# Performance work log

Measured on AMD Instinct MI355X. Metric: run time of the kernel, lower is better.

Reference implementation:

```python
import jax, jax.numpy as jnp
import numpy as np

N = 50000
E = 640000
NFEAT = 128
NHID = 128
ALPHA = 0.2  # leaky relu slope


def setup_inputs() -> dict:
    key = jax.random.key(0)
    k1, k2, k3, k4, k5 = jax.random.split(key, 5)
    x = jax.random.normal(k1, (N, NFEAT), dtype=jnp.float32)
    W = jax.random.normal(k2, (NFEAT, NHID), dtype=jnp.float32) * (1.0 / np.sqrt(NFEAT))
    a = jax.random.normal(k3, (1, 2 * NHID), dtype=jnp.float32) * 0.1
    # every node appears at least once as a source so rowsum > 0 (as in a real adjacency)
    src = jnp.concatenate([jnp.arange(N, dtype=jnp.int64 if jax.config.read('jax_enable_x64') else jnp.int32),
                           jax.random.randint(k4, (E - N,), 0, N)]).astype(jnp.int32)
    dst = jax.random.randint(k5, (E,), 0, N).astype(jnp.int32)
    edge_index = jnp.stack([src, dst], axis=0)
    return {"x": x, "W": W, "a": a, "edge_index": edge_index, "no_need_param": 0}


def reference(x, W, a, edge_index, no_need_param):
    # SpGraphAttentionLayer (concat=False), single head
    h = x @ W                                   # [N, nhid]
    src, dst = edge_index[0], edge_index[1]     # [E]
    nhid = W.shape[1]
    a1, a2 = a[0, :nhid], a[0, nhid:]
    # a @ cat(h[src], h[dst])  ==  h[src]@a1 + h[dst]@a2
    score = h[src] @ a1 + h[dst] @ a2           # [E]
    e = jnp.exp(-jax.nn.leaky_relu(score, ALPHA))
    n = x.shape[0]
    rowsum = jax.ops.segment_sum(e, src, num_segments=n)              # [N]
    h_prime = jax.ops.segment_sum(e[:, None] * h[dst], src, num_segments=n)  # [N, nhid]
    neighborhood_emb = h_prime / (rowsum[:, None] + 1e-16)
    # fused combine: elu(x @ W - neighborhood aggregation)
    mapped_fea = x @ W
    return jax.nn.elu(mapped_fea - neighborhood_emb)
```

## Files before the change

### kernel.cpp

```cpp
#include <hip/hip_runtime.h>
#include <hip/hip_fp16.h>
#include <math.h>

#define NFEAT 128
#define NHID  128
#define ALPHA 0.2f

typedef __attribute__((ext_vector_type(8))) short short8;
typedef __attribute__((ext_vector_type(4))) float f32x4;

__device__ inline unsigned int pack_bf16x2_rn(float x, float y) {
    unsigned int bx = __float_as_uint(x), by = __float_as_uint(y);
    bx += 0x7fffu + ((bx >> 16) & 1u);
    by += 0x7fffu + ((by >> 16) & 1u);
    return (bx >> 16) | (by & 0xffff0000u);
}

union Frag { unsigned int u[4]; uint4 v; short8 s; };

__global__ __launch_bounds__(256) void prep_wt_kernel(
    const float* __restrict__ W, unsigned int* __restrict__ Wtg)
{
    __shared__ float tile[32][33];
    const int t  = threadIdx.x;
    const int kt = blockIdx.x >> 2;
    const int nt = blockIdx.x & 3;

    {
        const int r = t >> 3, c = t & 7;
        const float4 v = *((const float4*)&W[(size_t)(kt * 32 + r) * NHID + nt * 32 + c * 4]);
        tile[r][c * 4 + 0] = v.x; tile[r][c * 4 + 1] = v.y;
        tile[r][c * 4 + 2] = v.z; tile[r][c * 4 + 3] = v.w;
    }
    __syncthreads();

    const int nn = t & 31;
    #pragma unroll
    for (int i = 0; i < 2; ++i) {
        const int kk = (t >> 5) * 2 + i;
        Wtg[(size_t)(nt * 32 + nn) * 64 + kt * 16 + kk] =
            pack_bf16x2_rn(tile[kk * 2][nn], tile[kk * 2 + 1][nn]);
    }
}

__global__ __launch_bounds__(256) void gemm_h_kernel(
    const float* __restrict__ x, const unsigned int* __restrict__ Wtg,
    const float* __restrict__ a, float* __restrict__ h,
    unsigned int* __restrict__ hbu,
    float* __restrict__ s1, float* __restrict__ s2, int n,
    const int* __restrict__ ei, int* __restrict__ hist, int E, int gemm_blocks)
{
    __shared__ unsigned int Wtu[128 * 64];

    const int t = threadIdx.x;

    if (blockIdx.x >= gemm_blocks) {
        const int E4   = E >> 2;
        const int nthr = (gridDim.x - gemm_blocks) << 8;
        const int g    = (blockIdx.x - gemm_blocks) * 256 + t;
        for (int idx = g; idx < E4; idx += nthr) {
            const int4 s4 = ((const int4*)ei)[idx];
            atomicAdd(&hist[s4.x], 1);
            atomicAdd(&hist[s4.y], 1);
            atomicAdd(&hist[s4.z], 1);
            atomicAdd(&hist[s4.w], 1);
        }
        for (int j = (E4 << 2) + g; j < E; j += nthr) atomicAdd(&hist[ei[j]], 1);
        return;
    }

    #pragma unroll
    for (int i = 0; i < 8; ++i) {
        const int u  = i * 256 + t;
        const uint4 v = ((const uint4*)Wtg)[u];
        const int nn = u >> 4, kc = u & 15;
        *((uint4*)&Wtu[nn * 64 + (kc ^ (nn & 15)) * 4]) = v;
    }

    const int w    = t >> 6;
    const int lane = t & 63;
    const int c    = lane & 15;
    const int quad = lane >> 4;

    const int rowbase = blockIdx.x * 64 + w * 16;

    int arow = rowbase + c; if (arow >= n) arow = n - 1;
    const float4* xp = (const float4*)(x + (size_t)arow * NFEAT);
    float4 xv[8];
    #pragma unroll
    for (int s = 0; s < 4; ++s) {
        xv[2 * s]     = xp[s * 8 + quad * 2];
        xv[2 * s + 1] = xp[s * 8 + quad * 2 + 1];
    }

    float a1v[8], a2v[8];
    #pragma unroll
    for (int tt = 0; tt < 8; ++tt) {
        a1v[tt] = a[tt * 16 + c];
        a2v[tt] = a[NHID + tt * 16 + c];
    }

    f32x4 acc[8];
    #pragma unroll
    for (int tt = 0; tt < 8; ++tt) acc[tt] = (f32x4){0.f, 0.f, 0.f, 0.f};

    __syncthreads();

    #pragma unroll
    for (int s = 0; s < 4; ++s) {
        Frag afr;
        afr.u[0] = pack_bf16x2_rn(xv[2 * s].x,     xv[2 * s].y);
        afr.u[1] = pack_bf16x2_rn(xv[2 * s].z,     xv[2 * s].w);
        afr.u[2] = pack_bf16x2_rn(xv[2 * s + 1].x, xv[2 * s + 1].y);
        afr.u[3] = pack_bf16x2_rn(xv[2 * s + 1].z, xv[2 * s + 1].w);
        const int kc = s * 4 + quad;
        #pragma unroll
        for (int tt = 0; tt < 8; ++tt) {
            Frag bfr;
            bfr.v = *((const uint4*)&Wtu[(tt * 16 + c) * 64 + (kc ^ c) * 4]);
            acc[tt] = __builtin_amdgcn_mfma_f32_16x16x32_bf16(
                afr.s, bfr.s, acc[tt], 0, 0, 0);
        }
    }

    #pragma unroll
    for (int r = 0; r < 4; ++r) {
        const int  row = rowbase + quad * 4 + r;
        const bool ok  = (row < n);
        float p1 = 0.f, p2 = 0.f;
        #pragma unroll
        for (int tt = 0; tt < 8; ++tt) {
            const float v = acc[tt][r];
            if (ok) h[(size_t)row * NHID + tt * 16 + c] = v;
            p1 = fmaf(v, a1v[tt], p1);
            p2 = fmaf(v, a2v[tt], p2);
        }
        #pragma unroll
        for (int p = 0; p < 4; ++p) {
            if (ok) hbu[(size_t)row * 64 + p * 16 + c] =
                pack_bf16x2_rn(acc[2 * p][r], acc[2 * p + 1][r]);
        }
        #pragma unroll
        for (int off = 1; off <= 8; off <<= 1) {
            p1 += __shfl_xor(p1, off, 64);
            p2 += __shfl_xor(p2, off, 64);
        }
        if (ok && c == 0) { s1[row] = p1; s2[row] = p2; }
    }
}

__global__ __launch_bounds__(256) void scan_block_kernel(
    const int* __restrict__ in, int* __restrict__ out, int* __restrict__ bsums, int n)
{
    __shared__ int s[256];
    const int tid = threadIdx.x;
    const int gid = blockIdx.x * 256 + tid;
    const int v = (gid < n) ? in[gid] : 0;
    s[tid] = v;
    __syncthreads();
    #pragma unroll
    for (int off = 1; off < 256; off <<= 1) {
        const int t2 = (tid >= off) ? s[tid - off] : 0;
        __syncthreads();
        s[tid] += t2;
        __syncthreads();
    }
    if (gid < n) out[gid] = s[tid] - v;
    if (tid == 255 && bsums) bsums[blockIdx.x] = s[255];
}

__global__ __launch_bounds__(256) void scan_add_kernel(
    int* __restrict__ row_ptr, int* __restrict__ cursor,
    const int* __restrict__ bsums_scan, int n, int E)
{
    const int gid = blockIdx.x * 256 + threadIdx.x;
    if (gid < n) {
        const int v = row_ptr[gid] + bsums_scan[gid >> 8];
        row_ptr[gid] = v;
        cursor[gid]  = v;
    }
    if (gid == 0) row_ptr[n] = E;
}

__global__ __launch_bounds__(256) void scatter_kernel(
    const int* __restrict__ ei, const float* __restrict__ s1,
    const float* __restrict__ s2, int* __restrict__ cursor,
    unsigned int* __restrict__ erec, int E)
{
    const int j = blockIdx.x * 256 + threadIdx.x;
    if (j >= E) return;
    const int src = ei[j];
    const int dst = ei[E + j];
    float s = s1[src] + s2[dst];
    s = (s > 0.f) ? s : ALPHA * s;
    const float ev = expf(-s);
    const unsigned int evh = (unsigned int)__half_as_ushort(__float2half(ev));
    const int pos = atomicAdd(&cursor[src], 1);
    erec[pos] = ((unsigned int)dst << 16) | evh;
}

__global__ __launch_bounds__(256) void aggregate_kernel(
    const int* __restrict__ row_ptr, const unsigned int* __restrict__ erec,
    const unsigned int* __restrict__ hbu, const float* __restrict__ h,
    float* __restrict__ out, int n)
{
    const int node = blockIdx.x * 16 + (threadIdx.x >> 4);
    const int l    = threadIdx.x & 15;
    if (node >= n) return;

    const int beg = row_ptr[node];
    const int end = row_ptr[node + 1];

    float acc[8];
    #pragma unroll
    for (int i = 0; i < 8; ++i) acc[i] = 0.f;
    float rs = 0.f;

    #define BL(x) __uint_as_float((x) << 16)
    #define BH(x) __uint_as_float((x) & 0xffff0000u)
    #define ACC4(u, ev)                                   \
        acc[0] = fmaf(ev, BL(u.x), acc[0]);               \
        acc[4] = fmaf(ev, BH(u.x), acc[4]);               \
        acc[1] = fmaf(ev, BL(u.y), acc[1]);               \
        acc[5] = fmaf(ev, BH(u.y), acc[5]);               \
        acc[2] = fmaf(ev, BL(u.z), acc[2]);               \
        acc[6] = fmaf(ev, BH(u.z), acc[6]);               \
        acc[3] = fmaf(ev, BL(u.w), acc[3]);               \
        acc[7] = fmaf(ev, BH(u.w), acc[7]);

    int e = beg;
    for (; e + 8 <= end; e += 8) {
        unsigned int rr[8];
        uint4 u[8];
        #pragma unroll
        for (int i = 0; i < 8; ++i) rr[i] = erec[e + i];
        #pragma unroll
        for (int i = 0; i < 8; ++i)
            u[i] = ((const uint4*)(hbu + (size_t)(rr[i] >> 16) * 64))[l];
        #pragma unroll
        for (int i = 0; i < 8; ++i) {
            const float ev = __half2float(__ushort_as_half((unsigned short)(rr[i] & 0xffffu)));
            ACC4(u[i], ev);
            rs += ev;
        }
    }
    for (; e + 2 <= end; e += 2) {
        const unsigned int r0 = erec[e], r1 = erec[e + 1];
        const uint4 u0 = ((const uint4*)(hbu + (size_t)(r0 >> 16) * 64))[l];
        const uint4 u1 = ((const uint4*)(hbu + (size_t)(r1 >> 16) * 64))[l];
        const float e0 = __half2float(__ushort_as_half((unsigned short)(r0 & 0xffffu)));
        const float e1 = __half2float(__ushort_as_half((unsigned short)(r1 & 0xffffu)));
        ACC4(u0, e0); ACC4(u1, e1);
        rs += e0 + e1;
    }
    if (e < end) {
        const unsigned int r0 = erec[e];
        const uint4 u0 = ((const uint4*)(hbu + (size_t)(r0 >> 16) * 64))[l];
        const float e0 = __half2float(__ushort_as_half((unsigned short)(r0 & 0xffffu)));
        ACC4(u0, e0);
        rs += e0;
    }
    #undef ACC4
    #undef BL
    #undef BH

    const float rinv = 1.0f / (rs + 1e-16f);
    const int p = l >> 2, q = l & 3;
    const float4* hp4 = (const float4*)(h + (size_t)node * NHID);
    const float4 ha = hp4[8 * p + q];
    const float4 hb = hp4[8 * p + 4 + q];
    float4 oa, ob;
    float z;
    z = ha.x - acc[0] * rinv; oa.x = (z > 0.f) ? z : (expf(z) - 1.f);
    z = ha.y - acc[1] * rinv; oa.y = (z > 0.f) ? z : (expf(z) - 1.f);
    z = ha.z - acc[2] * rinv; oa.z = (z > 0.f) ? z : (expf(z) - 1.f);
    z = ha.w - acc[3] * rinv; oa.w = (z > 0.f) ? z : (expf(z) - 1.f);
    z = hb.x - acc[4] * rinv; ob.x = (z > 0.f) ? z : (expf(z) - 1.f);
    z = hb.y - acc[5] * rinv; ob.y = (z > 0.f) ? z : (expf(z) - 1.f);
    z = hb.z - acc[6] * rinv; ob.z = (z > 0.f) ? z : (expf(z) - 1.f);
    z = hb.w - acc[7] * rinv; ob.w = (z > 0.f) ? z : (expf(z) - 1.f);
    float4* op = (float4*)(out + (size_t)node * NHID);
    op[8 * p + q]     = oa;
    op[8 * p + 4 + q] = ob;
}

extern "C" void kernel_launch(void* const* d_in, const int* in_sizes, int n_in,
                              void* d_out, int out_size, void* d_ws, size_t ws_size,
                              hipStream_t stream) {
    const float* x  = (const float*)d_in[0];
    const float* W  = (const float*)d_in[1];
    const float* a  = (const float*)d_in[2];
    const int*   ei = (const int*)d_in[3];

    const int n = in_sizes[0] / NFEAT;
    const int E = in_sizes[3] / 2;
    const int nb = (n + 255) / 256;

    float* out = (float*)d_out;

    float*        h     = (float*)d_ws;
    unsigned int* hbu   = (unsigned int*)(h + (size_t)n * NHID);
    float*        s1    = (float*)(hbu + (size_t)n * 64);
    float*        s2    = s1 + n;
    unsigned int* erec  = (unsigned int*)(s2 + n);
    unsigned int* Wtg   = erec + E;
    int*          hist  = (int*)(Wtg + 8192);
    int*          bsums = hist + n;
    int*          bsums_scan = bsums + 256;
    int*          row_ptr    = bsums_scan + 256;
    int*          cursor     = row_ptr + (n + 1);

    hipMemsetAsync(hist, 0, ((size_t)n + 256) * sizeof(int), stream);

    prep_wt_kernel<<<16, 256, 0, stream>>>(W, Wtg);

    const int gemm_blocks = (n + 63) / 64;
    const int hist_blocks = 128;
    gemm_h_kernel<<<gemm_blocks + hist_blocks, 256, 0, stream>>>(
        x, Wtg, a, h, hbu, s1, s2, n, ei, hist, E, gemm_blocks);

    scan_block_kernel<<<nb, 256, 0, stream>>>(hist, row_ptr, bsums, n);
    scan_block_kernel<<<1, 256, 0, stream>>>(bsums, bsums_scan, nullptr, 256);
    scan_add_kernel<<<nb, 256, 0, stream>>>(row_ptr, cursor, bsums_scan, n, E);

    scatter_kernel<<<(E + 255) / 256, 256, 0, stream>>>(ei, s1, s2, cursor, erec, E);

    aggregate_kernel<<<(n + 15) / 16, 256, 0, stream>>>(row_ptr, erec, hbu, h, out, n);
}
```

Measured before the change: 180.6 us.

## Fold memset into prep kernel, merge scans, aggregate two nodes per group

Replaces the hipMemsetAsync of the histogram with extra blocks in the weight-prep kernel and folds the second-level scan into scan_add, so each block rescans the block sums itself. This removes two launches from the chain. The aggregate kernel now has each 16-lane group handle two adjacent nodes in lockstep, four edges at a time, to get more gathers in flight per thread. The cost is predicated loads and wasted work when the two nodes' degrees differ, plus higher register pressure.

```diff
diff --git a/kernel.cpp b/kernel.cpp
--- a/kernel.cpp
+++ b/kernel.cpp
@@ -19,10 +19,23 @@
 union Frag { unsigned int u[4]; uint4 v; short8 s; };
 
 __global__ __launch_bounds__(256) void prep_wt_kernel(
-    const float* __restrict__ W, unsigned int* __restrict__ Wtg)
-{
+    const float* __restrict__ W, unsigned int* __restrict__ Wtg,
+    int* __restrict__ hist, int n)
+{
+    const int t = threadIdx.x;
+
+    if (blockIdx.x >= 16) {
+        const int n4     = n >> 2;
+        const int stride = (gridDim.x - 16) << 8;
+        int4* h4 = (int4*)hist;
+        for (int i = (blockIdx.x - 16) * 256 + t; i < n4; i += stride)
+            h4[i] = make_int4(0, 0, 0, 0);
+        for (int i = (n4 << 2) + (blockIdx.x - 16) * 256 + t; i < n; i += stride)
+            hist[i] = 0;
+        return;
+    }
+
     __shared__ float tile[32][33];
-    const int t  = threadIdx.x;
     const int kt = blockIdx.x >> 2;
     const int nt = blockIdx.x & 3;
 
@@ -166,16 +179,28 @@
         __syncthreads();
     }
     if (gid < n) out[gid] = s[tid] - v;
-    if (tid == 255 && bsums) bsums[blockIdx.x] = s[255];
+    if (tid == 255) bsums[blockIdx.x] = s[255];
 }
 
 __global__ __launch_bounds__(256) void scan_add_kernel(
     int* __restrict__ row_ptr, int* __restrict__ cursor,
-    const int* __restrict__ bsums_scan, int n, int E)
-{
-    const int gid = blockIdx.x * 256 + threadIdx.x;
+    const int* __restrict__ bsums, int n, int E, int nb)
+{
+    __shared__ int s[256];
+    const int tid = threadIdx.x;
+    s[tid] = (tid < nb) ? bsums[tid] : 0;
+    __syncthreads();
+    #pragma unroll
+    for (int off = 1; off < 256; off <<= 1) {
+        const int t2 = (tid >= off) ? s[tid - off] : 0;
+        __syncthreads();
+        s[tid] += t2;
+        __syncthreads();
+    }
+    const int offset = (blockIdx.x == 0) ? 0 : s[blockIdx.x - 1];
+    const int gid = blockIdx.x * 256 + tid;
     if (gid < n) {
-        const int v = row_ptr[gid] + bsums_scan[gid >> 8];
+        const int v = row_ptr[gid] + offset;
         row_ptr[gid] = v;
         cursor[gid]  = v;
     }
@@ -204,21 +229,30 @@
     const unsigned int* __restrict__ hbu, const float* __restrict__ h,
     float* __restrict__ out, int n)
 {
-    const int node = blockIdx.x * 16 + (threadIdx.x >> 4);
-    const int l    = threadIdx.x & 15;
-    if (node >= n) return;
-
-    const int beg = row_ptr[node];
-    const int end = row_ptr[node + 1];
-
-    float acc[8];
-    #pragma unroll
-    for (int i = 0; i < 8; ++i) acc[i] = 0.f;
-    float rs = 0.f;
+    const int grp = (blockIdx.x * 256 + threadIdx.x) >> 4;
+    const int l   = threadIdx.x & 15;
+    const int nodeA = grp * 2;
+    const int nodeB = nodeA + 1;
+    if (nodeA >= n) return;
+
+    const int begA = row_ptr[nodeA];
+    const int endA = row_ptr[nodeA + 1];
+    int begB = 0, endB = 0;
+    if (nodeB < n) { begB = endA; endB = row_ptr[nodeB + 1]; }
+
+    float accA[8], accB[8];
+    #pragma unroll
+    for (int i = 0; i < 8; ++i) { accA[i] = 0.f; accB[i] = 0.f; }
+    float rsA = 0.f, rsB = 0.f;
+
+    const uint4* hbu4 = (const uint4*)hbu;
+
+    const int dA = endA - begA, dB = endB - begB;
+    const int iters = max((dA + 3) >> 2, (dB + 3) >> 2);
 
     #define BL(x) __uint_as_float((x) << 16)
     #define BH(x) __uint_as_float((x) & 0xffff0000u)
-    #define ACC4(u, ev)                                   \
+    #define ACC4(acc, u, ev)                              \
         acc[0] = fmaf(ev, BL(u.x), acc[0]);               \
         acc[4] = fmaf(ev, BH(u.x), acc[4]);               \
         acc[1] = fmaf(ev, BL(u.y), acc[1]);               \
@@ -228,60 +262,72 @@
         acc[3] = fmaf(ev, BL(u.w), acc[3]);               \
         acc[7] = fmaf(ev, BH(u.w), acc[7]);
 
-    int e = beg;
-    for (; e + 8 <= end; e += 8) {
-        unsigned int rr[8];
-        uint4 u[8];
-        #pragma unroll
-        for (int i = 0; i < 8; ++i) rr[i] = erec[e + i];
-        #pragma unroll
-        for (int i = 0; i < 8; ++i)
-            u[i] = ((const uint4*)(hbu + (size_t)(rr[i] >> 16) * 64))[l];
-        #pragma unroll
-        for (int i = 0; i < 8; ++i) {
-            const float ev = __half2float(__ushort_as_half((unsigned short)(rr[i] & 0xffffu)));
-            ACC4(u[i], ev);
-            rs += ev;
-        }
-    }
-    for (; e + 2 <= end; e += 2) {
-        const unsigned int r0 = erec[e], r1 = erec[e + 1];
-        const uint4 u0 = ((const uint4*)(hbu + (size_t)(r0 >> 16) * 64))[l];
-        const uint4 u1 = ((const uint4*)(hbu + (size_t)(r1 >> 16) * 64))[l];
-        const float e0 = __half2float(__ushort_as_half((unsigned short)(r0 & 0xffffu)));
-        const float e1 = __half2float(__ushort_as_half((unsigned short)(r1 & 0xffffu)));
-        ACC4(u0, e0); ACC4(u1, e1);
-        rs += e0 + e1;
-    }
-    if (e < end) {
-        const unsigned int r0 = erec[e];
-        const uint4 u0 = ((const uint4*)(hbu + (size_t)(r0 >> 16) * 64))[l];
-        const float e0 = __half2float(__ushort_as_half((unsigned short)(r0 & 0xffffu)));
-        ACC4(u0, e0);
-        rs += e0;
+    for (int it = 0; it < iters; ++it) {
+        const int bA = begA + it * 4;
+        const int bB = begB + it * 4;
+        unsigned int rA[4], rB[4];
+        #pragma unroll
+        for (int j = 0; j < 4; ++j) rA[j] = (bA + j < endA) ? erec[bA + j] : 0u;
+        #pragma unroll
+        for (int j = 0; j < 4; ++j) rB[j] = (bB + j < endB) ? erec[bB + j] : 0u;
+        uint4 uA[4], uB[4];
+        #pragma unroll
+        for (int j = 0; j < 4; ++j) uA[j] = hbu4[(size_t)(rA[j] >> 16) * 16 + l];
+        #pragma unroll
+        for (int j = 0; j < 4; ++j) uB[j] = hbu4[(size_t)(rB[j] >> 16) * 16 + l];
+        #pragma unroll
+        for (int j = 0; j < 4; ++j) {
+            const float evA = __half2float(__ushort_as_half((unsigned short)(rA[j] & 0xffffu)));
+            const float evB = __half2float(__ushort_as_half((unsigned short)(rB[j] & 0xffffu)));
+            ACC4(accA, uA[j], evA);
+            ACC4(accB, uB[j], evB);
+            rsA += evA; rsB += evB;
+        }
     }
     #undef ACC4
     #undef BL
     #undef BH
 
-    const float rinv = 1.0f / (rs + 1e-16f);
     const int p = l >> 2, q = l & 3;
-    const float4* hp4 = (const float4*)(h + (size_t)node * NHID);
-    const float4 ha = hp4[8 * p + q];
-    const float4 hb = hp4[8 * p + 4 + q];
-    float4 oa, ob;
-    float z;
-    z = ha.x - acc[0] * rinv; oa.x = (z > 0.f) ? z : (expf(z) - 1.f);
-    z = ha.y - acc[1] * rinv; oa.y = (z > 0.f) ? z : (expf(z) - 1.f);
-    z = ha.z - acc[2] * rinv; oa.z = (z > 0.f) ? z : (expf(z) - 1.f);
-    z = ha.w - acc[3] * rinv; oa.w = (z > 0.f) ? z : (expf(z) - 1.f);
-    z = hb.x - acc[4] * rinv; ob.x = (z > 0.f) ? z : (expf(z) - 1.f);
-    z = hb.y - acc[5] * rinv; ob.y = (z > 0.f) ? z : (expf(z) - 1.f);
-    z = hb.z - acc[6] * rinv; ob.z = (z > 0.f) ? z : (expf(z) - 1.f);
-    z = hb.w - acc[7] * rinv; ob.w = (z > 0.f) ? z : (expf(z) - 1.f);
-    float4* op = (float4*)(out + (size_t)node * NHID);
-    op[8 * p + q]     = oa;
-    op[8 * p + 4 + q] = ob;
+
+    {
+        const float rinv = 1.0f / (rsA + 1e-16f);
+        const float4* hp4 = (const float4*)(h + (size_t)nodeA * NHID);
+        const float4 ha = hp4[8 * p + q];
+        const float4 hb = hp4[8 * p + 4 + q];
+        float4 oa, ob;
+        float z;
+        z = ha.x - accA[0] * rinv; oa.x = (z > 0.f) ? z : (expf(z) - 1.f);
+        z = ha.y - accA[1] * rinv; oa.y = (z > 0.f) ? z : (expf(z) - 1.f);
+        z = ha.z - accA[2] * rinv; oa.z = (z > 0.f) ? z : (expf(z) - 1.f);
+        z = ha.w - accA[3] * rinv; oa.w = (z > 0.f) ? z : (expf(z) - 1.f);
+        z = hb.x - accA[4] * rinv; ob.x = (z > 0.f) ? z : (expf(z) - 1.f);
+        z = hb.y - accA[5] * rinv; ob.y = (z > 0.f) ? z : (expf(z) - 1.f);
+        z = hb.z - accA[6] * rinv; ob.z = (z > 0.f) ? z : (expf(z) - 1.f);
+        z = hb.w - accA[7] * rinv; ob.w = (z > 0.f) ? z : (expf(z) - 1.f);
+        float4* op = (float4*)(out + (size_t)nodeA * NHID);
+        op[8 * p + q]     = oa;
+        op[8 * p + 4 + q] = ob;
+    }
+    if (nodeB < n) {
+        const float rinv = 1.0f / (rsB + 1e-16f);
+        const float4* hp4 = (const float4*)(h + (size_t)nodeB * NHID);
+        const float4 ha = hp4[8 * p + q];
+        const float4 hb = hp4[8 * p + 4 + q];
+        float4 oa, ob;
+        float z;
+        z = ha.x - accB[0] * rinv; oa.x = (z > 0.f) ? z : (expf(z) - 1.f);
+        z = ha.y - accB[1] * rinv; oa.y = (z > 0.f) ? z : (expf(z) - 1.f);
+        z = ha.z - accB[2] * rinv; oa.z = (z > 0.f) ? z : (expf(z) - 1.f);
+        z = ha.w - accB[3] * rinv; oa.w = (z > 0.f) ? z : (expf(z) - 1.f);
+        z = hb.x - accB[4] * rinv; ob.x = (z > 0.f) ? z : (expf(z) - 1.f);
+        z = hb.y - accB[5] * rinv; ob.y = (z > 0.f) ? z : (expf(z) - 1.f);
+        z = hb.z - accB[6] * rinv; ob.z = (z > 0.f) ? z : (expf(z) - 1.f);
+        z = hb.w - accB[7] * rinv; ob.w = (z > 0.f) ? z : (expf(z) - 1.f);
+        float4* op = (float4*)(out + (size_t)nodeB * NHID);
+        op[8 * p + q]     = oa;
+        op[8 * p + 4 + q] = ob;
+    }
 }
 
 extern "C" void kernel_launch(void* const* d_in, const int* in_sizes, int n_in,
@@ -306,13 +352,10 @@
     unsigned int* Wtg   = erec + E;
     int*          hist  = (int*)(Wtg + 8192);
     int*          bsums = hist + n;
-    int*          bsums_scan = bsums + 256;
-    int*          row_ptr    = bsums_scan + 256;
-    int*          cursor     = row_ptr + (n + 1);
-
-    hipMemsetAsync(hist, 0, ((size_t)n + 256) * sizeof(int), stream);
-
-    prep_wt_kernel<<<16, 256, 0, stream>>>(W, Wtg);
+    int*          row_ptr = bsums + 256;
+    int*          cursor  = row_ptr + (n + 1);
+
+    prep_wt_kernel<<<16 + 50, 256, 0, stream>>>(W, Wtg, hist, n);
 
     const int gemm_blocks = (n + 63) / 64;
     const int hist_blocks = 128;
@@ -320,10 +363,11 @@
         x, Wtg, a, h, hbu, s1, s2, n, ei, hist, E, gemm_blocks);
 
     scan_block_kernel<<<nb, 256, 0, stream>>>(hist, row_ptr, bsums, n);
-    scan_block_kernel<<<1, 256, 0, stream>>>(bsums, bsums_scan, nullptr, 256);
-    scan_add_kernel<<<nb, 256, 0, stream>>>(row_ptr, cursor, bsums_scan, n, E);
+    scan_add_kernel<<<nb, 256, 0, stream>>>(row_ptr, cursor, bsums, n, E, nb);
 
     scatter_kernel<<<(E + 255) / 256, 256, 0, stream>>>(ei, s1, s2, cursor, erec, E);
 
-    aggregate_kernel<<<(n + 15) / 16, 256, 0, stream>>>(row_ptr, erec, hbu, h, out, n);
-}
+    const int groups = (n + 1) / 2;
+    aggregate_kernel<<<(groups * 16 + 255) / 256, 256, 0, stream>>>(
+        row_ptr, erec, hbu, h, out, n);
+}
```

Result: no change. 182.9 us (+1.3%).

## Drop fp32 h buffer, fold memset and bsums scan into other kernels

Applied to the files above, without the earlier changes.

Stops writing the fp32 h matrix and instead reads the bf16 copy for the final subtraction, which removes about 25MB of writes plus reads. The hist zeroing moves from a memset into extra blocks of the prep kernel. The separate single-block scan of block sums is merged into scan_add, where every block redoes that small scan. The hbu layout changes to one uint4 store per row per lane. These steps remove two launches and a lot of memory traffic, at the cost of lower precision (bf16) for the x@W term in the output.

```diff
diff --git a/kernel.cpp b/kernel.cpp
--- a/kernel.cpp
+++ b/kernel.cpp
@@ -19,10 +19,23 @@
 union Frag { unsigned int u[4]; uint4 v; short8 s; };
 
 __global__ __launch_bounds__(256) void prep_wt_kernel(
-    const float* __restrict__ W, unsigned int* __restrict__ Wtg)
-{
+    const float* __restrict__ W, unsigned int* __restrict__ Wtg,
+    int* __restrict__ hist, int n)
+{
+    const int t = threadIdx.x;
+
+    if (blockIdx.x >= 16) {
+        const int n4     = n >> 2;
+        const int stride = (gridDim.x - 16) << 8;
+        int4* h4 = (int4*)hist;
+        for (int i = (blockIdx.x - 16) * 256 + t; i < n4; i += stride)
+            h4[i] = make_int4(0, 0, 0, 0);
+        for (int i = (n4 << 2) + (blockIdx.x - 16) * 256 + t; i < n; i += stride)
+            hist[i] = 0;
+        return;
+    }
+
     __shared__ float tile[32][33];
-    const int t  = threadIdx.x;
     const int kt = blockIdx.x >> 2;
     const int nt = blockIdx.x & 3;
 
@@ -45,8 +58,7 @@
 
 __global__ __launch_bounds__(256) void gemm_h_kernel(
     const float* __restrict__ x, const unsigned int* __restrict__ Wtg,
-    const float* __restrict__ a, float* __restrict__ h,
-    unsigned int* __restrict__ hbu,
+    const float* __restrict__ a, unsigned int* __restrict__ hbu,
     float* __restrict__ s1, float* __restrict__ s2, int n,
     const int* __restrict__ ei, int* __restrict__ hist, int E, int gemm_blocks)
 {
@@ -131,14 +143,16 @@
         #pragma unroll
         for (int tt = 0; tt < 8; ++tt) {
             const float v = acc[tt][r];
-            if (ok) h[(size_t)row * NHID + tt * 16 + c] = v;
             p1 = fmaf(v, a1v[tt], p1);
             p2 = fmaf(v, a2v[tt], p2);
         }
-        #pragma unroll
-        for (int p = 0; p < 4; ++p) {
-            if (ok) hbu[(size_t)row * 64 + p * 16 + c] =
-                pack_bf16x2_rn(acc[2 * p][r], acc[2 * p + 1][r]);
+        if (ok) {
+            uint4 pk;
+            pk.x = pack_bf16x2_rn(acc[0][r], acc[1][r]);
+            pk.y = pack_bf16x2_rn(acc[2][r], acc[3][r]);
+            pk.z = pack_bf16x2_rn(acc[4][r], acc[5][r]);
+            pk.w = pack_bf16x2_rn(acc[6][r], acc[7][r]);
+            *((uint4*)&hbu[(size_t)row * 64 + c * 4]) = pk;
         }
         #pragma unroll
         for (int off = 1; off <= 8; off <<= 1) {
@@ -166,16 +180,28 @@
         __syncthreads();
     }
     if (gid < n) out[gid] = s[tid] - v;
-    if (tid == 255 && bsums) bsums[blockIdx.x] = s[255];
+    if (tid == 255) bsums[blockIdx.x] = s[255];
 }
 
 __global__ __launch_bounds__(256) void scan_add_kernel(
     int* __restrict__ row_ptr, int* __restrict__ cursor,
-    const int* __restrict__ bsums_scan, int n, int E)
-{
-    const int gid = blockIdx.x * 256 + threadIdx.x;
+    const int* __restrict__ bsums, int n, int E, int nb)
+{
+    __shared__ int s[256];
+    const int tid = threadIdx.x;
+    s[tid] = (tid < nb) ? bsums[tid] : 0;
+    __syncthreads();
+    #pragma unroll
+    for (int off = 1; off < 256; off <<= 1) {
+        const int t2 = (tid >= off) ? s[tid - off] : 0;
+        __syncthreads();
+        s[tid] += t2;
+        __syncthreads();
+    }
+    const int offset = (blockIdx.x == 0) ? 0 : s[blockIdx.x - 1];
+    const int gid = blockIdx.x * 256 + tid;
     if (gid < n) {
-        const int v = row_ptr[gid] + bsums_scan[gid >> 8];
+        const int v = row_ptr[gid] + offset;
         row_ptr[gid] = v;
         cursor[gid]  = v;
     }
@@ -201,10 +227,9 @@
 
 __global__ __launch_bounds__(256) void aggregate_kernel(
     const int* __restrict__ row_ptr, const unsigned int* __restrict__ erec,
-    const unsigned int* __restrict__ hbu, const float* __restrict__ h,
-    float* __restrict__ out, int n)
-{
-    const int node = blockIdx.x * 16 + (threadIdx.x >> 4);
+    const unsigned int* __restrict__ hbu, float* __restrict__ out, int n)
+{
+    const int node = (blockIdx.x * 256 + threadIdx.x) >> 4;
     const int l    = threadIdx.x & 15;
     if (node >= n) return;
 
@@ -215,6 +240,8 @@
     #pragma unroll
     for (int i = 0; i < 8; ++i) acc[i] = 0.f;
     float rs = 0.f;
+
+    const uint4* hbu4 = (const uint4*)hbu;
 
     #define BL(x) __uint_as_float((x) << 16)
     #define BH(x) __uint_as_float((x) & 0xffff0000u)
@@ -236,7 +263,7 @@
         for (int i = 0; i < 8; ++i) rr[i] = erec[e + i];
         #pragma unroll
         for (int i = 0; i < 8; ++i)
-            u[i] = ((const uint4*)(hbu + (size_t)(rr[i] >> 16) * 64))[l];
+            u[i] = hbu4[(size_t)(rr[i] >> 16) * 16 + l];
         #pragma unroll
         for (int i = 0; i < 8; ++i) {
             const float ev = __half2float(__ushort_as_half((unsigned short)(rr[i] & 0xffffu)));
@@ -246,8 +273,8 @@
     }
     for (; e + 2 <= end; e += 2) {
         const unsigned int r0 = erec[e], r1 = erec[e + 1];
-        const uint4 u0 = ((const uint4*)(hbu + (size_t)(r0 >> 16) * 64))[l];
-        const uint4 u1 = ((const uint4*)(hbu + (size_t)(r1 >> 16) * 64))[l];
+        const uint4 u0 = hbu4[(size_t)(r0 >> 16) * 16 + l];
+        const uint4 u1 = hbu4[(size_t)(r1 >> 16) * 16 + l];
         const float e0 = __half2float(__ushort_as_half((unsigned short)(r0 & 0xffffu)));
         const float e1 = __half2float(__ushort_as_half((unsigned short)(r1 & 0xffffu)));
         ACC4(u0, e0); ACC4(u1, e1);
@@ -255,33 +282,27 @@
     }
     if (e < end) {
         const unsigned int r0 = erec[e];
-        const uint4 u0 = ((const uint4*)(hbu + (size_t)(r0 >> 16) * 64))[l];
+        const uint4 u0 = hbu4[(size_t)(r0 >> 16) * 16 + l];
         const float e0 = __half2float(__ushort_as_half((unsigned short)(r0 & 0xffffu)));
         ACC4(u0, e0);
         rs += e0;
     }
     #undef ACC4
+
+    const float rinv = 1.0f / (rs + 1e-16f);
+    const uint4 us = hbu4[(size_t)node * 16 + l];
+    float* op = out + (size_t)node * NHID + l;
+    float z;
+    z = BL(us.x) - acc[0] * rinv; op[0]   = (z > 0.f) ? z : (expf(z) - 1.f);
+    z = BH(us.x) - acc[4] * rinv; op[16]  = (z > 0.f) ? z : (expf(z) - 1.f);
+    z = BL(us.y) - acc[1] * rinv; op[32]  = (z > 0.f) ? z : (expf(z) - 1.f);
+    z = BH(us.y) - acc[5] * rinv; op[48]  = (z > 0.f) ? z : (expf(z) - 1.f);
+    z = BL(us.z) - acc[2] * rinv; op[64]  = (z > 0.f) ? z : (expf(z) - 1.f);
+    z = BH(us.z) - acc[6] * rinv; op[80]  = (z > 0.f) ? z : (expf(z) - 1.f);
+    z = BL(us.w) - acc[3] * rinv; op[96]  = (z > 0.f) ? z : (expf(z) - 1.f);
+    z = BH(us.w) - acc[7] * rinv; op[112] = (z > 0.f) ? z : (expf(z) - 1.f);
     #undef BL
     #undef BH
-
-    const float rinv = 1.0f / (rs + 1e-16f);
-    const int p = l >> 2, q = l & 3;
-    const float4* hp4 = (const float4*)(h + (size_t)node * NHID);
-    const float4 ha = hp4[8 * p + q];
-    const float4 hb = hp4[8 * p + 4 + q];
-    float4 oa, ob;
-    float z;
-    z = ha.x - acc[0] * rinv; oa.x = (z > 0.f) ? z : (expf(z) - 1.f);
-    z = ha.y - acc[1] * rinv; oa.y = (z > 0.f) ? z : (expf(z) - 1.f);
-    z = ha.z - acc[2] * rinv; oa.z = (z > 0.f) ? z : (expf(z) - 1.f);
-    z = ha.w - acc[3] * rinv; oa.w = (z > 0.f) ? z : (expf(z) - 1.f);
-    z = hb.x - acc[4] * rinv; ob.x = (z > 0.f) ? z : (expf(z) - 1.f);
-    z = hb.y - acc[5] * rinv; ob.y = (z > 0.f) ? z : (expf(z) - 1.f);
-    z = hb.z - acc[6] * rinv; ob.z = (z > 0.f) ? z : (expf(z) - 1.f);
-    z = hb.w - acc[7] * rinv; ob.w = (z > 0.f) ? z : (expf(z) - 1.f);
-    float4* op = (float4*)(out + (size_t)node * NHID);
-    op[8 * p + q]     = oa;
-    op[8 * p + 4 + q] = ob;
 }
 
 extern "C" void kernel_launch(void* const* d_in, const int* in_sizes, int n_in,
@@ -298,32 +319,28 @@
 
     float* out = (float*)d_out;
 
-    float*        h     = (float*)d_ws;
-    unsigned int* hbu   = (unsigned int*)(h + (size_t)n * NHID);
-    float*        s1    = (float*)(hbu + (size_t)n * 64);
-    float*        s2    = s1 + n;
-    unsigned int* erec  = (unsigned int*)(s2 + n);
-    unsigned int* Wtg   = erec + E;
-    int*          hist  = (int*)(Wtg + 8192);
-    int*          bsums = hist + n;
-    int*          bsums_scan = bsums + 256;
-    int*          row_ptr    = bsums_scan + 256;
-    int*          cursor     = row_ptr + (n + 1);
-
-    hipMemsetAsync(hist, 0, ((size_t)n + 256) * sizeof(int), stream);
-
-    prep_wt_kernel<<<16, 256, 0, stream>>>(W, Wtg);
+    unsigned int* hbu    = (unsigned int*)d_ws;
+    float*        s1     = (float*)(hbu + (size_t)n * 64);
+    float*        s2     = s1 + n;
+    unsigned int* erec   = (unsigned int*)(s2 + n);
+    unsigned int* Wtg    = erec + E;
+    int*          hist   = (int*)(Wtg + 8192);
+    int*          bsums  = hist + n;
+    int*          row_ptr = bsums + 256;
+    int*          cursor  = row_ptr + (n + 1);
+
+    prep_wt_kernel<<<16 + 50, 256, 0, stream>>>(W, Wtg, hist, n);
 
     const int gemm_blocks = (n + 63) / 64;
     const int hist_blocks = 128;
     gemm_h_kernel<<<gemm_blocks + hist_blocks, 256, 0, stream>>>(
-        x, Wtg, a, h, hbu, s1, s2, n, ei, hist, E, gemm_blocks);
+        x, Wtg, a, hbu, s1, s2, n, ei, hist, E, gemm_blocks);
 
     scan_block_kernel<<<nb, 256, 0, stream>>>(hist, row_ptr, bsums, n);
-    scan_block_kernel<<<1, 256, 0, stream>>>(bsums, bsums_scan, nullptr, 256);
-    scan_add_kernel<<<nb, 256, 0, stream>>>(row_ptr, cursor, bsums_scan, n, E);
+    scan_add_kernel<<<nb, 256, 0, stream>>>(row_ptr, cursor, bsums, n, E, nb);
 
     scatter_kernel<<<(E + 255) / 256, 256, 0, stream>>>(ei, s1, s2, cursor, erec, E);
 
-    aggregate_kernel<<<(n + 15) / 16, 256, 0, stream>>>(row_ptr, erec, hbu, h, out, n);
-}
+    aggregate_kernel<<<((size_t)n * 16 + 255) / 256, 256, 0, stream>>>(
+        row_ptr, erec, hbu, out, n);
+}
```

After: 176.2 us (median of 2 runs). -2.4%, faster.
